# Kernel tuning notes

Measured on AMD Instinct MI355X. Metric: run time of the kernel, lower is better.

## Reference

```python
import jax, jax.numpy as jnp
import numpy as np

# irreps layout: in/out = 32x0e + 8x1o  (dim 32 + 24 = 56), sh = 1x0e + 1x1o (dim 4)
NS, NV = 32, 8
N_NODES, N_EDGES, N_EDGE_FEAT, HIDDEN = 10000, 100000, 64, 64
W_NUMEL = NS*NS + NS*NV + NV*NV + NV*NS  # 1600
EPS = 1e-5
# path normalization (e3nn-style 'component'/'element'):
# fan_in into 0e output = 32 (0x0 path) + 8 (1x1 path) = 40; same for 1o output.
INV40 = 1.0 / np.sqrt(40.0)            # paths with trivial/identity CG net factor
INV120 = 1.0 / np.sqrt(120.0)          # paths with w3j = delta/sqrt(3) extra factor


def setup_inputs() -> dict:
    key = jax.random.key(0)
    ks = jax.random.split(key, 12)
    node_attr = jax.random.normal(ks[0], (N_NODES, 56), dtype=jnp.float32)
    edge_attr = jax.random.normal(ks[1], (N_EDGES, N_EDGE_FEAT), dtype=jnp.float32)
    edge_sh = jax.random.normal(ks[2], (N_EDGES, 4), dtype=jnp.float32)
    edge_index = jax.random.randint(ks[3], (2, N_EDGES), 0, N_NODES, dtype=jnp.int64)
    s1 = 1.0 / np.sqrt(N_EDGE_FEAT)
    s2 = 1.0 / np.sqrt(HIDDEN)
    fc1_w = jax.random.normal(ks[4], (N_EDGE_FEAT, HIDDEN), dtype=jnp.float32) * s1
    fc1_b = jnp.zeros((HIDDEN,), dtype=jnp.float32)
    fc2_w = jax.random.normal(ks[5], (HIDDEN, W_NUMEL), dtype=jnp.float32) * s2
    fc2_b = jnp.zeros((W_NUMEL,), dtype=jnp.float32)
    bn_gamma0 = jnp.ones((NS,), dtype=jnp.float32)
    bn_beta0 = jnp.zeros((NS,), dtype=jnp.float32)
    bn_gamma1 = jnp.ones((NV,), dtype=jnp.float32)
    return dict(node_attr=node_attr, edge_attr=edge_attr, edge_sh=edge_sh,
                edge_index=edge_index, fc1_w=fc1_w, fc1_b=fc1_b,
                fc2_w=fc2_w, fc2_b=fc2_b, bn_gamma0=bn_gamma0,
                bn_beta0=bn_beta0, bn_gamma1=bn_gamma1)


def _forward(node_attr, edge_attr, edge_sh, fc1_w, fc1_b, fc2_w, fc2_b,
             bn_gamma0, bn_beta0, bn_gamma1, edge_index):
    E = edge_attr.shape[0]
    N = node_attr.shape[0]
    edge_src, edge_dst = edge_index[0], edge_index[1]

    # edge MLP -> per-edge tensor-product weights [E, 1600]
    h = jax.nn.relu(edge_attr @ fc1_w + fc1_b)
    w = h @ fc2_w + fc2_b
    o1 = NS * NS            # 0e x 0e -> 0e
    o2 = o1 + NS * NV       # 0e x 1o -> 1o
    o3 = o2 + NV * NV       # 1o x 0e -> 1o
    w00 = w[:, :o1].reshape(E, NS, NS)
    w01 = w[:, o1:o2].reshape(E, NS, NV)
    w10 = w[:, o2:o3].reshape(E, NV, NV)
    w11 = w[:, o3:].reshape(E, NV, NS)

    # gather node features at destination, split into scalar / vector irreps
    x = node_attr[edge_dst]                  # [E, 56]
    x0 = x[:, :NS]                           # [E, 32] scalars
    x1 = x[:, NS:].reshape(E, NV, 3)         # [E, 8, 3] l=1 vectors
    s0 = edge_sh[:, 0]                       # [E]
    s1 = edge_sh[:, 1:4]                     # [E, 3]

    # Clebsch-Gordan paths (w3j(1,1,0)=w3j(1,0,1)=w3j(0,1,1)=delta/sqrt(3))
    out0 = jnp.einsum('eu,euw->ew', x0 * s0[:, None], w00) * INV40 \
         + jnp.einsum('eui,ei,euw->ew', x1, s1, w11) * INV120
    out1 = jnp.einsum('eu,ei,euw->ewi', x0, s1, w01) * INV40 \
         + jnp.einsum('eui,euw->ewi', x1 * s0[:, None, None], w10) * INV40
    tp_out = jnp.concatenate([out0, out1.reshape(E, NV * 3)], axis=-1)  # [E, 56]

    # scatter-mean over edge_src
    sums = jax.ops.segment_sum(tp_out, edge_src, num_segments=N)
    cnt = jax.ops.segment_sum(jnp.ones((E,), tp_out.dtype), edge_src, num_segments=N)
    out = sums / jnp.maximum(cnt, 1.0)[:, None]

    # residual (in_dim == out_dim, pad is a no-op)
    out = out + node_attr

    # e3nn-style BatchNorm (training statistics, reduce='mean')
    sc = out[:, :NS]
    vec = out[:, NS:].reshape(N, NV, 3)
    m = sc.mean(axis=0)
    sc_c = sc - m
    var = (sc_c ** 2).mean(axis=0)
    sc_n = sc_c * jax.lax.rsqrt(var + EPS) * bn_gamma0 + bn_beta0
    vnorm = (vec ** 2).mean(axis=-1).mean(axis=0)          # [NV]
    vec_n = vec * (jax.lax.rsqrt(vnorm + EPS) * bn_gamma1)[None, :, None]
    return jnp.concatenate([sc_n, vec_n.reshape(N, NV * 3)], axis=-1)


def reference(node_attr, edge_attr, edge_sh, edge_index, fc1_w, fc1_b,
              fc2_w, fc2_b, bn_gamma0, bn_beta0, bn_gamma1):
    return _forward(node_attr, edge_attr, edge_sh, fc1_w, fc1_b, fc2_w,
                    fc2_b, bn_gamma0, bn_beta0, bn_gamma1, edge_index)
```

## Files before the change

kernel.cpp:

```cpp
#include <hip/hip_runtime.h>

typedef __attribute__((ext_vector_type(4))) float f32x4;
typedef __attribute__((ext_vector_type(2))) float f32x2;
typedef __attribute__((ext_vector_type(8))) short bf16x8;

#define NEDGE 100000
#define NNODE 10000
#define INV40f 0.15811388300841897f
#define INV120f 0.09128709291752769f

__device__ inline short f2bf(float f) {
    unsigned u = __builtin_bit_cast(unsigned, f);
    u = (u + 0x7fffu + ((u >> 16) & 1u)) >> 16;
    return (short)u;
}

__device__ __forceinline__ float bperm(int byteIdx, float v) {
    return __builtin_bit_cast(float,
        __builtin_amdgcn_ds_bpermute(byteIdx, __builtin_bit_cast(int, v)));
}

__device__ __forceinline__ void stage16(const void* gsrc, void* ldst) {
    __builtin_amdgcn_global_load_lds(
        (const __attribute__((address_space(1))) unsigned*)gsrc,
        (__attribute__((address_space(3))) unsigned*)(unsigned long long)(uintptr_t)ldst,
        16, 0, 0);
}

#define MFMA16(A,B,C) __builtin_amdgcn_mfma_f32_16x16x32_bf16((A),(B),(C),0,0,0)

__global__ __launch_bounds__(256) void prep(const float* __restrict__ fc1_w,
                                            const float* __restrict__ fc2_w,
                                            short* __restrict__ fc1_wt,
                                            short* __restrict__ fc2_wt,
                                            float* __restrict__ stats,
                                            int* __restrict__ hist) {
    const int b = blockIdx.x, t = threadIdx.x;
    if (b < 25) {
        __shared__ short tile[64 * 66];
        const int c0 = b * 64;
        #pragma unroll
        for (int rep = 0; rep < 16; rep++) {
            const int idx = rep * 256 + t;
            const int k = idx >> 6, c = idx & 63;
            tile[k * 66 + c] = f2bf(fc2_w[(size_t)k * 1600 + c0 + c]);
        }
        __syncthreads();
        #pragma unroll
        for (int rep = 0; rep < 16; rep++) {
            const int idx = rep * 256 + t;
            const int c = idx >> 6, k = idx & 63;
            fc2_wt[(size_t)(c0 + c) * 64 + k] = tile[k * 66 + c];
        }
    } else if (b == 25) {
        #pragma unroll
        for (int rep = 0; rep < 16; rep++) {
            const int i = rep * 256 + t;
            fc1_wt[(i & 63) * 64 + (i >> 6)] = f2bf(fc1_w[i]);
        }
    } else if (b == 26) {
        if (t < 72) stats[t] = 0.0f;
    } else {
        const int i = (b - 27) * 256 + t;
        if (i < NNODE) hist[i] = 0;
    }
}

__global__ __launch_bounds__(512, 4) void edge_fused(
    const float* __restrict__ node_attr,
    const float* __restrict__ edge_attr,
    const float* __restrict__ edge_sh,
    const int*   __restrict__ edge_index,
    const float* __restrict__ fc1_b,
    const float* __restrict__ fc2_b,
    const short* __restrict__ fc1_wt,
    const short* __restrict__ fc2_wt,
    float* __restrict__ tp_out,
    int*   __restrict__ hist)
{
    __shared__ __align__(16) char lds[57600];
    char* cbA = lds;
    char* cbB = lds + 16384;
    float* bias_s = (float*)(lds + 51200);

    const int tid  = threadIdx.x;
    const int wid  = tid >> 6;
    const int wtid = tid & 63;
    const int l15  = wtid & 15;
    const int lg   = wtid >> 4;
    const int lg4  = lg * 4;
    const int e0   = blockIdx.x * 128 + wid * 16;
    const bool active = (e0 < NEDGE);

    char*  h_s = lds + 32768 + wid * 2048;
    float* shb = (float*)(lds + 49152 + wid * 256);

#define STAGE1(CH, BUF, J) do { \
        const int _o = (wid * 2 + (J)) * 1024 + wtid * 16; \
        const int _g = _o ^ (((_o >> 7) & 7) << 4); \
        stage16((const char*)fc2_wt + (CH) * 16384 + _g, (BUF) + (wid * 2 + (J)) * 1024); \
    } while (0)
#define STAGE_FULL(CH, BUF) do { STAGE1(CH, BUF, 0); STAGE1(CH, BUF, 1); } while (0)

    STAGE_FULL(0, cbA);

    if (tid < 400) {
        *(f32x4*)(bias_s + tid * 4) = *(const f32x4*)(fc2_b + tid * 4);
    }

    int dst_r = 0;
    if (active && wtid < 16) {
        dst_r = edge_index[NEDGE + e0 + wtid];
        const int src = edge_index[e0 + wtid];
        const f32x4 sh_r = *(const f32x4*)(edge_sh + (size_t)(e0 + wtid) * 4);
        atomicAdd(&hist[src], 1);
        *(f32x4*)(shb + wtid * 4) = sh_r;
    }

    bf16x8 ha0, ha1;
    f32x4 shv = {0.f, 0.f, 0.f, 0.f};
    float c00r[8], cb1r[8], c10r[6], c11r[2];
    int vidx[4];
    #pragma unroll
    for (int g = 0; g < 4; g++) vidx[g] = (g * 16 + l15) * 4;

    if (active) {
        const float* pa = edge_attr + (size_t)(e0 + l15) * 64 + lg * 8;
        const f32x4 va0 = *(const f32x4*)(pa);
        const f32x4 va1 = *(const f32x4*)(pa + 4);
        const f32x4 va2 = *(const f32x4*)(pa + 32);
        const f32x4 va3 = *(const f32x4*)(pa + 36);

        const int dstm = __shfl(dst_r, l15, 64);
        const float* nap = node_attr + (size_t)dstm * 56;
        const f32x4 x0a = *(const f32x4*)(nap + lg * 8);
        const f32x4 x0b = *(const f32x4*)(nap + lg * 8 + 4);
        const f32x2 x1a = *(const f32x2*)(nap + 32 + lg * 6);
        const f32x2 x1b = *(const f32x2*)(nap + 34 + lg * 6);
        const f32x2 x1c = *(const f32x2*)(nap + 36 + lg * 6);
        shv = *(const f32x4*)(shb + l15 * 4);

        const float s0 = shv[0];
        #pragma unroll
        for (int j = 0; j < 4; j++) {
            cb1r[j]     = INV40f * x0a[j];
            cb1r[4 + j] = INV40f * x0b[j];
            c00r[j]     = s0 * cb1r[j];
            c00r[4 + j] = s0 * cb1r[4 + j];
        }
        const float i40s0 = INV40f * s0;
        c10r[0] = i40s0 * x1a[0]; c10r[1] = i40s0 * x1a[1]; c10r[2] = i40s0 * x1b[0];
        c10r[3] = i40s0 * x1b[1]; c10r[4] = i40s0 * x1c[0]; c10r[5] = i40s0 * x1c[1];
        c11r[0] = INV120f * (x1a[0]*shv[1] + x1a[1]*shv[2] + x1b[0]*shv[3]);
        c11r[1] = INV120f * (x1b[1]*shv[1] + x1c[0]*shv[2] + x1c[1]*shv[3]);

        bf16x8 a0, a1;
        #pragma unroll
        for (int i = 0; i < 4; i++) {
            a0[i] = f2bf(va0[i]); a0[4+i] = f2bf(va1[i]);
            a1[i] = f2bf(va2[i]); a1[4+i] = f2bf(va3[i]);
        }
        #pragma unroll
        for (int nf0 = 0; nf0 < 4; nf0++) {
            const bf16x8 b0 = *(const bf16x8*)(fc1_wt + (nf0*16 + l15)*64 + lg*8);
            const bf16x8 b1 = *(const bf16x8*)(fc1_wt + (nf0*16 + l15)*64 + 32 + lg*8);
            const float bias = fc1_b[nf0*16 + l15];
            f32x4 c = {bias, bias, bias, bias};
            c = MFMA16(a0, b0, c);
            c = MFMA16(a1, b1, c);
            #pragma unroll
            for (int reg = 0; reg < 4; reg++) {
                const int row = lg4 + reg;
                *(short*)(h_s + ((row*128 + (nf0*16 + l15)*2) ^ ((row & 7) << 4))) =
                    f2bf(fmaxf(c[reg], 0.0f));
            }
        }
        ha0 = *(const bf16x8*)(h_s + ((l15*128 +      lg*16) ^ ((l15 & 7) << 4)));
        ha1 = *(const bf16x8*)(h_s + ((l15*128 + 64 + lg*16) ^ ((l15 & 7) << 4)));
    }

    const int hswz = (l15 & 7) << 4;
    const int ro0 = (l15 * 128 + lg * 16) ^ hswz;
    const int ro1 = (l15 * 128 + lg * 16 + 64) ^ hswz;
    const int usel = lg >> 1;
    float acc0[2][4] = {{0,0,0,0},{0,0,0,0}};
    float ab1[4] = {0,0,0,0};
    float b2v[12] = {};

    auto cons_w00 = [&](const char* cb, int ch) {
        bf16x8 pb0[3], pb1[3]; f32x4 pc[3];
        #pragma unroll
        for (int k = 0; k < 3; k++) {
            pb0[k] = *(const bf16x8*)(cb + k * 2048 + ro0);
            pb1[k] = *(const bf16x8*)(cb + k * 2048 + ro1);
            pc[k]  = *(const f32x4*)(bias_s + (ch * 8 + k) * 16 + lg4);
        }
        #pragma unroll
        for (int i = 0; i < 8; i++) {
            const int s = i % 3;
            const bf16x8 b0 = pb0[s], b1 = pb1[s];
            f32x4 c = pc[s];
            if (i + 3 < 8) {
                pb0[s] = *(const bf16x8*)(cb + (i + 3) * 2048 + ro0);
                pb1[s] = *(const bf16x8*)(cb + (i + 3) * 2048 + ro1);
                pc[s]  = *(const f32x4*)(bias_s + (ch * 8 + i + 3) * 16 + lg4);
            }
            c = MFMA16(b0, ha0, c);
            c = MFMA16(b1, ha1, c);
            const int nf = ch * 8 + i;
            const int u = nf >> 1, hi = nf & 1;
            const float cv = bperm(vidx[u >> 3], c00r[u & 7]);
            #pragma unroll
            for (int reg = 0; reg < 4; reg++) acc0[hi][reg] += cv * c[reg];
        }
    };
    auto cons_w01 = [&](const char* cb, int rbase) {
        bf16x8 pb0[3], pb1[3]; f32x4 pc[3];
        #pragma unroll
        for (int k = 0; k < 3; k++) {
            pb0[k] = *(const bf16x8*)(cb + k * 2048 + ro0);
            pb1[k] = *(const bf16x8*)(cb + k * 2048 + ro1);
            pc[k]  = *(const f32x4*)(bias_s + (64 + rbase + k) * 16 + lg4);
        }
        #pragma unroll
        for (int i = 0; i < 8; i++) {
            const int s = i % 3;
            const bf16x8 b0 = pb0[s], b1 = pb1[s];
            f32x4 c = pc[s];
            if (i + 3 < 8) {
                pb0[s] = *(const bf16x8*)(cb + (i + 3) * 2048 + ro0);
                pb1[s] = *(const bf16x8*)(cb + (i + 3) * 2048 + ro1);
                pc[s]  = *(const f32x4*)(bias_s + (64 + rbase + i + 3) * 16 + lg4);
            }
            c = MFMA16(b0, ha0, c);
            c = MFMA16(b1, ha1, c);
            const int nfl_r = rbase + i;
            const int r0 = (2 * nfl_r) & 7, g = nfl_r >> 2;
            const float e0v = bperm(vidx[g], cb1r[r0]);
            const float e1v = bperm(vidx[g], cb1r[r0 + 1]);
            const float cv = usel ? e1v : e0v;
            #pragma unroll
            for (int reg = 0; reg < 4; reg++) ab1[reg] += cv * c[reg];
        }
    };
    auto cons_w10 = [&](const char* cb, int fb) {
        bf16x8 pb0[2], pb1[2]; f32x4 pc[2];
        #pragma unroll
        for (int k = 0; k < 2; k++) {
            pb0[k] = *(const bf16x8*)(cb + (fb + k) * 2048 + ro0);
            pb1[k] = *(const bf16x8*)(cb + (fb + k) * 2048 + ro1);
            pc[k]  = *(const f32x4*)(bias_s + (80 + k) * 16 + lg4);
        }
        #pragma unroll
        for (int i = 0; i < 4; i++) {
            const int s = i % 2;
            const bf16x8 b0 = pb0[s], b1 = pb1[s];
            f32x4 c = pc[s];
            if (i + 2 < 4) {
                pb0[s] = *(const bf16x8*)(cb + (fb + i + 2) * 2048 + ro0);
                pb1[s] = *(const bf16x8*)(cb + (fb + i + 2) * 2048 + ro1);
                pc[s]  = *(const f32x4*)(bias_s + (80 + i + 2) * 16 + lg4);
            }
            c = MFMA16(b0, ha0, c);
            c = MFMA16(b1, ha1, c);
            #pragma unroll
            for (int k = 0; k < 3; k++) {
                const float e0v = bperm(vidx[i], c10r[k]);
                const float e1v = bperm(vidx[i], c10r[3 + k]);
                const float cv = usel ? e1v : e0v;
                #pragma unroll
                for (int reg = 0; reg < 4; reg++) b2v[reg * 3 + k] += cv * c[reg];
            }
        }
    };
    auto cons_w11_4 = [&](const char* cb, int fb, int ridx0) {
        bf16x8 pb0[2], pb1[2]; f32x4 pc[2];
        #pragma unroll
        for (int k = 0; k < 2; k++) {
            pb0[k] = *(const bf16x8*)(cb + (fb + k) * 2048 + ro0);
            pb1[k] = *(const bf16x8*)(cb + (fb + k) * 2048 + ro1);
            pc[k]  = *(const f32x4*)(bias_s + (84 + ridx0 + k) * 16 + lg4);
        }
        #pragma unroll
        for (int i = 0; i < 4; i++) {
            const int s = i % 2;
            const bf16x8 b0 = pb0[s], b1 = pb1[s];
            f32x4 c = pc[s];
            if (i + 2 < 4) {
                pb0[s] = *(const bf16x8*)(cb + (fb + i + 2) * 2048 + ro0);
                pb1[s] = *(const bf16x8*)(cb + (fb + i + 2) * 2048 + ro1);
                pc[s]  = *(const f32x4*)(bias_s + (84 + ridx0 + i + 2) * 16 + lg4);
            }
            c = MFMA16(b0, ha0, c);
            c = MFMA16(b1, ha1, c);
            const int ridx = ridx0 + i;
            const int up = ridx >> 1, hi = ridx & 1;
            const float cv = bperm(vidx[up >> 1], c11r[up & 1]);
            #pragma unroll
            for (int reg = 0; reg < 4; reg++) acc0[hi][reg] += cv * c[reg];
        }
    };
    auto cons_w11_8 = [&](const char* cb, int ridx0) {
        bf16x8 pb0[3], pb1[3]; f32x4 pc[3];
        #pragma unroll
        for (int k = 0; k < 3; k++) {
            pb0[k] = *(const bf16x8*)(cb + k * 2048 + ro0);
            pb1[k] = *(const bf16x8*)(cb + k * 2048 + ro1);
            pc[k]  = *(const f32x4*)(bias_s + (84 + ridx0 + k) * 16 + lg4);
        }
        #pragma unroll
        for (int i = 0; i < 8; i++) {
            const int s = i % 3;
            const bf16x8 b0 = pb0[s], b1 = pb1[s];
            f32x4 c = pc[s];
            if (i + 3 < 8) {
                pb0[s] = *(const bf16x8*)(cb + (i + 3) * 2048 + ro0);
                pb1[s] = *(const bf16x8*)(cb + (i + 3) * 2048 + ro1);
                pc[s]  = *(const f32x4*)(bias_s + (84 + ridx0 + i + 3) * 16 + lg4);
            }
            c = MFMA16(b0, ha0, c);
            c = MFMA16(b1, ha1, c);
            const int ridx = ridx0 + i;
            const int up = ridx >> 1, hi = ridx & 1;
            const float cv = bperm(vidx[up >> 1], c11r[up & 1]);
            #pragma unroll
            for (int reg = 0; reg < 4; reg++) acc0[hi][reg] += cv * c[reg];
        }
    };

    __syncthreads();
    STAGE_FULL(1,  cbB); if (active) cons_w00(cbA, 0); __syncthreads();
    STAGE_FULL(2,  cbA); if (active) cons_w00(cbB, 1); __syncthreads();
    STAGE_FULL(3,  cbB); if (active) cons_w00(cbA, 2); __syncthreads();
    STAGE_FULL(4,  cbA); if (active) cons_w00(cbB, 3); __syncthreads();
    STAGE_FULL(5,  cbB); if (active) cons_w00(cbA, 4); __syncthreads();
    STAGE_FULL(6,  cbA); if (active) cons_w00(cbB, 5); __syncthreads();
    STAGE_FULL(7,  cbB); if (active) cons_w00(cbA, 6); __syncthreads();
    STAGE_FULL(8,  cbA); if (active) cons_w00(cbB, 7); __syncthreads();
    STAGE_FULL(9,  cbB); if (active) cons_w01(cbA, 0); __syncthreads();
    STAGE_FULL(10, cbA); if (active) cons_w01(cbB, 8); __syncthreads();
    STAGE_FULL(11, cbB); if (active) { cons_w10(cbA, 0); cons_w11_4(cbA, 4, 0); } __syncthreads();
    STAGE_FULL(12, cbA); if (active) cons_w11_8(cbB, 4); __syncthreads();
                         if (active) cons_w11_4(cbA, 0, 12);

    if (!active) return;

    float* orow = tp_out + (size_t)(e0 + l15) * 56;
    {
        const f32x4 o0 = {acc0[0][0], acc0[0][1], acc0[0][2], acc0[0][3]};
        const f32x4 o1 = {acc0[1][0], acc0[1][1], acc0[1][2], acc0[1][3]};
        *(f32x4*)(orow + lg4)      = o0;
        *(f32x4*)(orow + 16 + lg4) = o1;
    }
    #pragma unroll
    for (int reg = 0; reg < 4; reg++) ab1[reg] += __shfl_xor(ab1[reg], 32, 64);
    #pragma unroll
    for (int m = 0; m < 12; m++) b2v[m] += __shfl_xor(b2v[m], 32, 64);
    if (lg < 2) {
        float ov[12];
        #pragma unroll
        for (int reg = 0; reg < 4; reg++) {
            ov[reg*3 + 0] = shv[1] * ab1[reg] + b2v[reg*3 + 0];
            ov[reg*3 + 1] = shv[2] * ab1[reg] + b2v[reg*3 + 1];
            ov[reg*3 + 2] = shv[3] * ab1[reg] + b2v[reg*3 + 2];
        }
        float* p1 = orow + 32 + lg * 12;
        *(f32x4*)(p1)     = f32x4{ov[0], ov[1], ov[2],  ov[3]};
        *(f32x4*)(p1 + 4) = f32x4{ov[4], ov[5], ov[6],  ov[7]};
        *(f32x4*)(p1 + 8) = f32x4{ov[8], ov[9], ov[10], ov[11]};
    }
#undef STAGE1
#undef STAGE_FULL
}

__global__ __launch_bounds__(256) void scan_hist(const int* __restrict__ hist,
                                                 int* __restrict__ offsets,
                                                 int* __restrict__ cursor) {
    __shared__ int wsum[4];
    const int t = threadIdx.x;
    const int lane = t & 63;
    const int w = t >> 6;
    const int n0 = t * 40;
    int s = 0;
    if (n0 < NNODE) {
        for (int j = 0; j < 40; j++) s += hist[n0 + j];
    }
    int incl = s;
    #pragma unroll
    for (int d = 1; d < 64; d <<= 1) {
        const int v = __shfl_up(incl, d, 64);
        if (lane >= d) incl += v;
    }
    if (lane == 63) wsum[w] = incl;
    __syncthreads();
    int base = 0;
    for (int ww = 0; ww < 4; ww++) base += (ww < w) ? wsum[ww] : 0;
    if (n0 < NNODE) {
        int run = base + incl - s;
        for (int j = 0; j < 40; j++) {
            const int h = hist[n0 + j];
            offsets[n0 + j] = run; cursor[n0 + j] = run; run += h;
        }
    }
    if (t == 0) offsets[NNODE] = NEDGE;
}

__global__ __launch_bounds__(256) void fill_perm(const int* __restrict__ edge_index,
                                                 int* __restrict__ cursor,
                                                 int* __restrict__ perm) {
    const int e = blockIdx.x * 256 + threadIdx.x;
    if (e < NEDGE) {
        const int s = edge_index[e];
        const int p = atomicAdd(&cursor[s], 1);
        perm[p] = e;
    }
}

__global__ __launch_bounds__(256) void node_agg(
    const float* __restrict__ tp_out, const int* __restrict__ offsets,
    const int* __restrict__ perm,
    const float* __restrict__ node_attr, float* __restrict__ out,
    float* __restrict__ stats)
{
    __shared__ float part[72];
    const int tid = threadIdx.x;
    if (tid < 72) part[tid] = 0.0f;
    __syncthreads();
    const int n = blockIdx.x * 16 + (tid >> 4);
    const int q = tid & 15;
    if (n < NNODE && q < 14) {
        const int st = offsets[n], en = offsets[n + 1];
        f32x4 acc = {0.f, 0.f, 0.f, 0.f};
        for (int r = st; r < en; r++)
            acc += *(const f32x4*)(tp_out + (size_t)perm[r] * 56 + q * 4);
        const float inv = 1.0f / fmaxf((float)(en - st), 1.0f);
        const int c0 = q * 4;
        const f32x4 res = *(const f32x4*)(node_attr + (size_t)n * 56 + c0);
        f32x4 val;
        #pragma unroll
        for (int j = 0; j < 4; j++) {
            val[j] = acc[j] * inv + res[j];
            const int c = c0 + j;
            if (c < 32) {
                atomicAdd(&part[c], val[j]);
                atomicAdd(&part[32 + c], val[j] * val[j]);
            } else {
                atomicAdd(&part[64 + (c - 32) / 3], val[j] * val[j]);
            }
        }
        *(f32x4*)(out + (size_t)n * 56 + c0) = val;
    }
    __syncthreads();
    if (tid < 72) unsafeAtomicAdd(&stats[tid], part[tid]);
}

__global__ __launch_bounds__(256) void node_norm(
    float* __restrict__ out, const float* __restrict__ stats,
    const float* __restrict__ g0, const float* __restrict__ b0,
    const float* __restrict__ g1)
{
    const int id = blockIdx.x * 256 + threadIdx.x;
    if (id >= NNODE * 56) return;
    const int c = id % 56;
    float val = out[id];
    if (c < 32) {
        const float m   = stats[c]      * (1.0f / NNODE);
        const float ex2 = stats[32 + c] * (1.0f / NNODE);
        const float var = ex2 - m * m;
        val = (val - m) * rsqrtf(var + 1e-5f) * g0[c] + b0[c];
    } else {
        const int v = (c - 32) / 3;
        const float vn = stats[64 + v] * (1.0f / (3.0f * NNODE));
        val = val * rsqrtf(vn + 1e-5f) * g1[v];
    }
    out[id] = val;
}

extern "C" void kernel_launch(void* const* d_in, const int* in_sizes, int n_in,
                              void* d_out, int out_size, void* d_ws, size_t ws_size,
                              hipStream_t stream) {
    const float* node_attr = (const float*)d_in[0];
    const float* edge_attr = (const float*)d_in[1];
    const float* edge_sh   = (const float*)d_in[2];
    const int*   edge_index= (const int*)  d_in[3];
    const float* fc1_w     = (const float*)d_in[4];
    const float* fc1_b     = (const float*)d_in[5];
    const float* fc2_w     = (const float*)d_in[6];
    const float* fc2_b     = (const float*)d_in[7];
    const float* g0        = (const float*)d_in[8];
    const float* b0        = (const float*)d_in[9];
    const float* g1        = (const float*)d_in[10];
    float* out = (float*)d_out;

    char* ws = (char*)d_ws;
    float* stats   = (float*)(ws + 0);
    int*   hist    = (int*)  (ws + 288);
    int*   offsets = (int*)  (ws + 40288);
    int*   cursor  = (int*)  (ws + 80320);
    int*   perm    = (int*)  (ws + 120320);
    short* fc1_wt  = (short*)(ws + 520320);
    short* fc2_wt  = (short*)(ws + 528512);
    float* tp_out  = (float*)(ws + 733312);

    prep<<<67, 256, 0, stream>>>(fc1_w, fc2_w, fc1_wt, fc2_wt, stats, hist);
    edge_fused<<<782, 512, 0, stream>>>(node_attr, edge_attr, edge_sh, edge_index,
                                        fc1_b, fc2_b, fc1_wt, fc2_wt, tp_out, hist);
    scan_hist<<<1, 256, 0, stream>>>(hist, offsets, cursor);
    fill_perm<<<391, 256, 0, stream>>>(edge_index, cursor, perm);
    node_agg<<<625, 256, 0, stream>>>(tp_out, offsets, perm, node_attr, out, stats);
    node_norm<<<2188, 256, 0, stream>>>(out, stats, g0, b0, g1);
}
```

Baseline: 103.7 us.

## Build CSR before edge kernel and write tp_out directly in sorted order

The source-node histogram and scan now run before the edge kernel, inside prep. The edge kernel takes its write slot from an atomic on the cursor array and stores each edge's 56 outputs into a CSR-ordered row padded to 64 floats, zero-filling the padding. This removes the fill_perm kernel and the indirect perm gather in node_agg, which now reads contiguous rows. LDS shrinks by aliasing the hidden-activation buffer onto the second weight buffer, and zeroing moves to a memset. The cost is a larger workspace, a scattered write pattern from the edge kernel, and extra padding bytes, with a fallback to the old path when the workspace is too small.

Measured after the change: 105.0 us. No clear change (+1.2%).

```diff
diff --git a/kernel.cpp b/kernel.cpp
--- a/kernel.cpp
+++ b/kernel.cpp
@@ -31,9 +31,9 @@
 
 __global__ __launch_bounds__(256) void prep(const float* __restrict__ fc1_w,
                                             const float* __restrict__ fc2_w,
+                                            const int* __restrict__ edge_index,
                                             short* __restrict__ fc1_wt,
                                             short* __restrict__ fc2_wt,
-                                            float* __restrict__ stats,
                                             int* __restrict__ hist) {
     const int b = blockIdx.x, t = threadIdx.x;
     if (b < 25) {
@@ -58,14 +58,13 @@
             const int i = rep * 256 + t;
             fc1_wt[(i & 63) * 64 + (i >> 6)] = f2bf(fc1_w[i]);
         }
-    } else if (b == 26) {
-        if (t < 72) stats[t] = 0.0f;
     } else {
-        const int i = (b - 27) * 256 + t;
-        if (i < NNODE) hist[i] = 0;
-    }
-}
-
+        const int e = (b - 26) * 256 + t;
+        if (e < NEDGE) atomicAdd(&hist[edge_index[e]], 1);
+    }
+}
+
+template<bool CSR>
 __global__ __launch_bounds__(512, 4) void edge_fused(
     const float* __restrict__ node_attr,
     const float* __restrict__ edge_attr,
@@ -76,12 +75,12 @@
     const short* __restrict__ fc1_wt,
     const short* __restrict__ fc2_wt,
     float* __restrict__ tp_out,
-    int*   __restrict__ hist)
+    int*   __restrict__ histcur)
 {
-    __shared__ __align__(16) char lds[57600];
+    __shared__ __align__(16) char lds[41216];
     char* cbA = lds;
     char* cbB = lds + 16384;
-    float* bias_s = (float*)(lds + 51200);
+    float* bias_s = (float*)(lds + 34816);
 
     const int tid  = threadIdx.x;
     const int wid  = tid >> 6;
@@ -92,8 +91,8 @@
     const int e0   = blockIdx.x * 128 + wid * 16;
     const bool active = (e0 < NEDGE);
 
-    char*  h_s = lds + 32768 + wid * 2048;
-    float* shb = (float*)(lds + 49152 + wid * 256);
+    char*  h_s = cbB + wid * 2048;
+    float* shb = (float*)(lds + 32768 + wid * 256);
 
 #define STAGE1(CH, BUF, J) do { \
         const int _o = (wid * 2 + (J)) * 1024 + wtid * 16; \
@@ -108,14 +107,15 @@
         *(f32x4*)(bias_s + tid * 4) = *(const f32x4*)(fc2_b + tid * 4);
     }
 
-    int dst_r = 0;
+    int dst_r = 0, slot_r = 0;
     if (active && wtid < 16) {
         dst_r = edge_index[NEDGE + e0 + wtid];
         const int src = edge_index[e0 + wtid];
         const f32x4 sh_r = *(const f32x4*)(edge_sh + (size_t)(e0 + wtid) * 4);
-        atomicAdd(&hist[src], 1);
+        slot_r = atomicAdd(&histcur[src], 1);
         *(f32x4*)(shb + wtid * 4) = sh_r;
     }
+    const int p_e = __shfl(slot_r, l15, 64);
 
     bf16x8 ha0, ha1;
     f32x4 shv = {0.f, 0.f, 0.f, 0.f};
@@ -345,7 +345,8 @@
 
     if (!active) return;
 
-    float* orow = tp_out + (size_t)(e0 + l15) * 56;
+    float* orow = CSR ? (tp_out + (size_t)p_e * 64)
+                      : (tp_out + (size_t)(e0 + l15) * 56);
     {
         const f32x4 o0 = {acc0[0][0], acc0[0][1], acc0[0][2], acc0[0][3]};
         const f32x4 o1 = {acc0[1][0], acc0[1][1], acc0[1][2], acc0[1][3]};
@@ -368,6 +369,8 @@
         *(f32x4*)(p1)     = f32x4{ov[0], ov[1], ov[2],  ov[3]};
         *(f32x4*)(p1 + 4) = f32x4{ov[4], ov[5], ov[6],  ov[7]};
         *(f32x4*)(p1 + 8) = f32x4{ov[8], ov[9], ov[10], ov[11]};
+    } else if (CSR) {
+        *(f32x4*)(orow + 56 + (lg - 2) * 4) = f32x4{0.f, 0.f, 0.f, 0.f};
     }
 #undef STAGE1
 #undef STAGE_FULL
@@ -416,6 +419,7 @@
     }
 }
 
+template<bool PERM>
 __global__ __launch_bounds__(256) void node_agg(
     const float* __restrict__ tp_out, const int* __restrict__ offsets,
     const int* __restrict__ perm,
@@ -431,8 +435,10 @@
     if (n < NNODE && q < 14) {
         const int st = offsets[n], en = offsets[n + 1];
         f32x4 acc = {0.f, 0.f, 0.f, 0.f};
-        for (int r = st; r < en; r++)
-            acc += *(const f32x4*)(tp_out + (size_t)perm[r] * 56 + q * 4);
+        for (int r = st; r < en; r++) {
+            const size_t row = PERM ? (size_t)perm[r] * 56 : (size_t)r * 64;
+            acc += *(const f32x4*)(tp_out + row + q * 4);
+        }
         const float inv = 1.0f / fmaxf((float)(en - st), 1.0f);
         const int c0 = q * 4;
         const f32x4 res = *(const f32x4*)(node_attr + (size_t)n * 56 + c0);
@@ -502,11 +508,22 @@
     short* fc2_wt  = (short*)(ws + 528512);
     float* tp_out  = (float*)(ws + 733312);
 
-    prep<<<67, 256, 0, stream>>>(fc1_w, fc2_w, fc1_wt, fc2_wt, stats, hist);
-    edge_fused<<<782, 512, 0, stream>>>(node_attr, edge_attr, edge_sh, edge_index,
-                                        fc1_b, fc2_b, fc1_wt, fc2_wt, tp_out, hist);
-    scan_hist<<<1, 256, 0, stream>>>(hist, offsets, cursor);
-    fill_perm<<<391, 256, 0, stream>>>(edge_index, cursor, perm);
-    node_agg<<<625, 256, 0, stream>>>(tp_out, offsets, perm, node_attr, out, stats);
+    const bool csr = (ws_size >= 733312ull + 100000ull * 64 * 4);
+
+    hipMemsetAsync(ws, 0, 40288, stream);
+    if (csr) {
+        prep<<<417, 256, 0, stream>>>(fc1_w, fc2_w, edge_index, fc1_wt, fc2_wt, hist);
+        scan_hist<<<1, 256, 0, stream>>>(hist, offsets, cursor);
+        edge_fused<true><<<782, 512, 0, stream>>>(node_attr, edge_attr, edge_sh, edge_index,
+                                                  fc1_b, fc2_b, fc1_wt, fc2_wt, tp_out, cursor);
+        node_agg<false><<<625, 256, 0, stream>>>(tp_out, offsets, nullptr, node_attr, out, stats);
+    } else {
+        prep<<<26, 256, 0, stream>>>(fc1_w, fc2_w, edge_index, fc1_wt, fc2_wt, hist);
+        edge_fused<false><<<782, 512, 0, stream>>>(node_attr, edge_attr, edge_sh, edge_index,
+                                                   fc1_b, fc2_b, fc1_wt, fc2_wt, tp_out, hist);
+        scan_hist<<<1, 256, 0, stream>>>(hist, offsets, cursor);
+        fill_perm<<<391, 256, 0, stream>>>(edge_index, cursor, perm);
+        node_agg<true><<<625, 256, 0, stream>>>(tp_out, offsets, perm, node_attr, out, stats);
+    }
     node_norm<<<2188, 256, 0, stream>>>(out, stats, g0, b0, g1);
 }
```
